# Kernel tuning notes

Hardware: AMD Instinct MI355X
Metric: run time of the kernel (lower is better)

Reference implementation:

```python
import jax, jax.numpy as jnp
import numpy as np
import math

B, T, C, H = 2, 1024, 1024, 16
D = C // H


def setup_inputs() -> dict:
    key = jax.random.key(0)
    ks = jax.random.split(key, 7)
    scale = 1.0 / math.sqrt(C)
    q = jax.random.normal(ks[0], (B, T, C), dtype=jnp.float32)
    k = jax.random.normal(ks[1], (B, T, C), dtype=jnp.float32)
    v = jax.random.normal(ks[2], (B, T, C), dtype=jnp.float32)
    # causal mask, True = masked out (matches create_causal_mask)
    mask = jnp.triu(jnp.ones((T, T), dtype=bool), k=1)[None, None]
    Wk = jax.random.normal(ks[3], (C, C), dtype=jnp.float32) * scale
    bk = jax.random.normal(ks[4], (C,), dtype=jnp.float32) * scale
    Wc = jax.random.normal(ks[5], (C, C), dtype=jnp.float32) * scale
    bc = jax.random.normal(ks[6], (C,), dtype=jnp.float32) * scale
    return {"q": q, "k": k, "v": v, "mask": mask, "Wk": Wk, "bk": bk, "Wc": Wc, "bc": bc}


def reference(q, k, v, mask, Wk, bk, Wc, bc):
    # NOTE: original module uses self.k_attn for ALL of q, k, v (q_attn/v_attn unused).
    qB, qT, qC = q.shape
    kT = k.shape[1]
    qp = (q @ Wk.T + bk).reshape(qB, qT, H, D).transpose(0, 2, 1, 3)  # [B,H,Tq,D]
    kp = (k @ Wk.T + bk).reshape(qB, kT, H, D).transpose(0, 2, 1, 3)  # [B,H,Tk,D]
    vp = (v @ Wk.T + bk).reshape(qB, kT, H, D).transpose(0, 2, 1, 3)  # [B,H,Tk,D]
    att = jnp.einsum('bhqd,bhkd->bhqk', qp, kp) * (1.0 / math.sqrt(D))
    att = jnp.where(mask, -jnp.inf, att)
    att = jax.nn.softmax(att, axis=-1)
    y = jnp.einsum('bhqk,bhkd->bhqd', att, vp)
    y = y.transpose(0, 2, 1, 3).reshape(qB, qT, qC)
    return y @ Wc.T + bc
```

## Files before the change

kernel.cpp:

```cpp
#include <hip/hip_runtime.h>

#define T_DIM 1024
#define C_DIM 1024
#define H_DIM 16
#define D_DIM 64
#define KD    1024

typedef short  short8  __attribute__((ext_vector_type(8)));
typedef short  short4v __attribute__((ext_vector_type(4)));
typedef float  f32x4   __attribute__((ext_vector_type(4)));

__device__ __forceinline__ float bf2f(short s) {
  return __uint_as_float(((unsigned)(unsigned short)s) << 16);
}
__device__ __forceinline__ short f2bf(float f) {
  unsigned u = __float_as_uint(f);
  u += 0x7fffu + ((u >> 16) & 1u);
  return (short)(u >> 16);
}
__device__ __forceinline__ unsigned pk2(float lo, float hi) {
  return ((unsigned)(unsigned short)f2bf(lo)) | (((unsigned)(unsigned short)f2bf(hi)) << 16);
}

__device__ __forceinline__ void gl2lds16(const short* g, short* l) {
  __builtin_amdgcn_global_load_lds(
      (const __attribute__((address_space(1))) unsigned int*)(const void*)g,
      (__attribute__((address_space(3))) unsigned int*)(void*)l,
      16, 0, 0);
}

__device__ __forceinline__ short8 ldfrag(const void* p, size_t off, int isf32) {
  if (isf32) {
    const float* q = (const float*)p + off;
    f32x4 lo = *(const f32x4*)q;
    f32x4 hi = *(const f32x4*)(q + 4);
    short8 r;
#pragma unroll
    for (int j = 0; j < 4; ++j) { r[j] = f2bf(lo[j]); r[j + 4] = f2bf(hi[j]); }
    return r;
  }
  return *(const short8*)((const short*)p + off);
}
__device__ __forceinline__ float ldbias(const void* b, int i, int isf32) {
  return isf32 ? ((const float*)b)[i] : bf2f(((const short*)b)[i]);
}

__device__ __forceinline__ int detect_f32_inblock(const unsigned* w, int lane) {
  int c = 0;
#pragma unroll
  for (int i = 0; i < 4; ++i) {
    unsigned e = (w[lane * 4 + i] >> 7) & 0xffu;
    c += (e >= 110u && e <= 135u) ? 1 : 0;
  }
#pragma unroll
  for (int off = 32; off; off >>= 1) c += __shfl_xor(c, off);
  return (c < 128) ? 1 : 0;
}

#define SZE  ((size_t)2 * T_DIM * C_DIM)
#define QN   ((size_t)2097152)
#define WN   ((size_t)1048576)
#define BN   ((size_t)1024)
#define CVT_TOT (3 * QN + 2 * WN + 2 * BN)

__global__ __launch_bounds__(256) void cvt_k(const void* __restrict__ q,
                                             const void* __restrict__ k,
                                             const void* __restrict__ v,
                                             const void* __restrict__ wk,
                                             const void* __restrict__ wc,
                                             const void* __restrict__ bk,
                                             const void* __restrict__ bc,
                                             short* __restrict__ dst)
{
  const int lane = threadIdx.x & 63;
  const int f = detect_f32_inblock((const unsigned*)q, lane);

  const size_t idx = (size_t)blockIdx.x * 1024 + threadIdx.x * 4;
  if (idx >= CVT_TOT) return;
  const void* src;
  size_t loc;
  if      (idx <     QN)          { src = q;  loc = idx; }
  else if (idx < 2 * QN)          { src = k;  loc = idx - QN; }
  else if (idx < 3 * QN)          { src = v;  loc = idx - 2 * QN; }
  else if (idx < 3 * QN + WN)     { src = wk; loc = idx - 3 * QN; }
  else if (idx < 3 * QN + 2 * WN) { src = wc; loc = idx - 3 * QN - WN; }
  else if (idx < 3 * QN + 2 * WN + BN) { src = bk; loc = idx - 3 * QN - 2 * WN; }
  else                            { src = bc; loc = idx - 3 * QN - 2 * WN - BN; }

  short4v o;
  if (f) {
    f32x4 x = *(const f32x4*)((const float*)src + loc);
#pragma unroll
    for (int j = 0; j < 4; ++j) o[j] = f2bf(x[j]);
  } else {
    o = *(const short4v*)((const short*)src + loc);
  }
  *(short4v*)(dst + idx) = o;
}

__device__ __forceinline__ void stage8x8(const short* gsrc, short* S, int R0,
                                         int lane, int koff) {
  const int rw = R0 + (lane >> 3);
  const int q  = (lane & 7) ^ (rw & 7);
  gl2lds16(gsrc + (size_t)rw * KD + koff + q * 8, &S[R0 * 64]);
}
__device__ __forceinline__ short8 fragread64(const short* S, int row, int chunk) {
  const int sl = (row << 3) + (chunk ^ (row & 7));
  return *(const short8*)&S[sl << 3];
}

__global__ __launch_bounds__(256) void gemm_qkv_a(const short* __restrict__ X0,
                                                  const short* __restrict__ X1,
                                                  const short* __restrict__ X2,
                                                  const short* __restrict__ Wv,
                                                  const short* __restrict__ Bv,
                                                  short* __restrict__ outv)
{
  const int tid  = threadIdx.x;
  const int lane = tid & 63;
  const int wave = tid >> 6;
  const int col16 = lane & 15;
  const int quad  = lane >> 4;

  const int f   = blockIdx.x;
  const int xcd = f & 7;
  const int j   = f >> 3;
  const int mt  = xcd * 6 + (j % 6);
  const int ct  = j / 6;
  const int m0 = mt * 128;
  const int c0 = ct * 64;

  const int src = m0 >> 11;
  const short* Xv = (src == 0) ? X0 : (src == 1) ? X1 : X2;
  const int arow = m0 & 2047;
  const bool isv = (src == 2);
  short* outb = outv + (size_t)src * SZE;

  __shared__ short As[2][128 * 64];
  __shared__ short Bs[2][64 * 64];

  const short* Xg = Xv + (size_t)arow * KD;
  const short* Wg = Wv + (size_t)c0 * KD;

  f32x4 acc[2][4] = {};

  stage8x8(Xg, As[0], wave * 32,      lane, 0);
  stage8x8(Xg, As[0], wave * 32 + 8,  lane, 0);
  stage8x8(Xg, As[0], wave * 32 + 16, lane, 0);
  stage8x8(Xg, As[0], wave * 32 + 24, lane, 0);
  stage8x8(Wg, Bs[0], wave * 16,      lane, 0);
  stage8x8(Wg, Bs[0], wave * 16 + 8,  lane, 0);
  __syncthreads();

  int cur = 0;
  for (int k0 = 0; k0 < KD; k0 += 64) {
    if (k0 + 64 < KD) {
      short* An = As[cur ^ 1];
      short* Bn = Bs[cur ^ 1];
      stage8x8(Xg, An, wave * 32,      lane, k0 + 64);
      stage8x8(Xg, An, wave * 32 + 8,  lane, k0 + 64);
      stage8x8(Xg, An, wave * 32 + 16, lane, k0 + 64);
      stage8x8(Xg, An, wave * 32 + 24, lane, k0 + 64);
      stage8x8(Wg, Bn, wave * 16,      lane, k0 + 64);
      stage8x8(Wg, Bn, wave * 16 + 8,  lane, k0 + 64);
    }

    const short* Ac = As[cur];
    const short* Bc = Bs[cur];
#pragma unroll
    for (int kk = 0; kk < 2; ++kk) {
      short8 fx[2], fw[4];
#pragma unroll
      for (int i = 0; i < 2; ++i)
        fx[i] = fragread64(Ac, wave * 32 + i * 16 + col16, kk * 4 + quad);
#pragma unroll
      for (int jj = 0; jj < 4; ++jj)
        fw[jj] = fragread64(Bc, jj * 16 + col16, kk * 4 + quad);

      if (isv) {
#pragma unroll
        for (int i = 0; i < 2; ++i)
#pragma unroll
          for (int jj = 0; jj < 4; ++jj)
            acc[i][jj] = __builtin_amdgcn_mfma_f32_16x16x32_bf16(fx[i], fw[jj], acc[i][jj], 0, 0, 0);
      } else {
#pragma unroll
        for (int i = 0; i < 2; ++i)
#pragma unroll
          for (int jj = 0; jj < 4; ++jj)
            acc[i][jj] = __builtin_amdgcn_mfma_f32_16x16x32_bf16(fw[jj], fx[i], acc[i][jj], 0, 0, 0);
      }
    }

    __syncthreads();
    cur ^= 1;
  }

  if (isv) {
#pragma unroll
    for (int i = 0; i < 2; ++i) {
#pragma unroll
      for (int jj = 0; jj < 4; ++jj) {
        const int c  = c0 + jj * 16 + col16;
        const int t0 = arow + wave * 32 + i * 16 + quad * 4;
        const float bv = bf2f(Bv[c]);
        short4v pk;
#pragma unroll
        for (int r = 0; r < 4; ++r) pk[r] = f2bf(acc[i][jj][r] + bv);
        const int bb = t0 >> 10, t = t0 & 1023, h = c >> 6, d = c & 63;
        size_t off = (size_t)((bb * H_DIM + h) * D_DIM + d) * T_DIM + t;
        *(short4v*)(outb + off) = pk;
      }
    }
  } else {
#pragma unroll
    for (int i = 0; i < 2; ++i) {
#pragma unroll
      for (int jj = 0; jj < 4; ++jj) {
        const int m  = arow + wave * 32 + i * 16 + col16;
        const int cb = c0 + jj * 16 + quad * 4;
        short4v bv4 = *(const short4v*)(Bv + cb);
        short4v pk;
#pragma unroll
        for (int r = 0; r < 4; ++r) pk[r] = f2bf(acc[i][jj][r] + bf2f(bv4[r]));
        const int bb = m >> 10, t = m & 1023, h = cb >> 6, d = cb & 63;
        size_t off = ((size_t)(bb * H_DIM + h) << 16) + (size_t)t * D_DIM + d;
        *(short4v*)(outb + off) = pk;
      }
    }
  }
}

__global__ __launch_bounds__(256) void gemm_out_a(const short* __restrict__ Xb,
                                                  const short* __restrict__ Wv,
                                                  const short* __restrict__ Bv,
                                                  float* __restrict__ outv)
{
  const int tid  = threadIdx.x;
  const int lane = tid & 63;
  const int wave = tid >> 6;
  const int col16 = lane & 15;
  const int quad  = lane >> 4;
  const int wm = wave & 1;
  const int wn = wave >> 1;

  const int f   = blockIdx.x;
  const int xcd = f & 7;
  const int j   = f >> 3;
  const int mt  = xcd * 4 + (j % 4);
  const int ct  = j / 4;
  const int m0 = mt * 64;
  const int c0 = ct * 64;

  __shared__ short As[2][64 * 64];
  __shared__ short Bs[2][64 * 64];

  const short* Xg = Xb + (size_t)m0 * KD;
  const short* Wg = Wv + (size_t)c0 * KD;

  f32x4 acc[2][2] = {};

  stage8x8(Xg, As[0], wave * 16,     lane, 0);
  stage8x8(Xg, As[0], wave * 16 + 8, lane, 0);
  stage8x8(Wg, Bs[0], wave * 16,     lane, 0);
  stage8x8(Wg, Bs[0], wave * 16 + 8, lane, 0);
  __syncthreads();

  int cur = 0;
  for (int k0 = 0; k0 < KD; k0 += 64) {
    if (k0 + 64 < KD) {
      short* An = As[cur ^ 1];
      short* Bn = Bs[cur ^ 1];
      stage8x8(Xg, An, wave * 16,     lane, k0 + 64);
      stage8x8(Xg, An, wave * 16 + 8, lane, k0 + 64);
      stage8x8(Wg, Bn, wave * 16,     lane, k0 + 64);
      stage8x8(Wg, Bn, wave * 16 + 8, lane, k0 + 64);
    }

    const short* Ac = As[cur];
    const short* Bc = Bs[cur];
#pragma unroll
    for (int kk = 0; kk < 2; ++kk) {
      short8 fx[2], fw[2];
#pragma unroll
      for (int i = 0; i < 2; ++i)
        fx[i] = fragread64(Ac, wm * 32 + i * 16 + col16, kk * 4 + quad);
#pragma unroll
      for (int jj = 0; jj < 2; ++jj)
        fw[jj] = fragread64(Bc, wn * 32 + jj * 16 + col16, kk * 4 + quad);

#pragma unroll
      for (int i = 0; i < 2; ++i)
#pragma unroll
        for (int jj = 0; jj < 2; ++jj)
          acc[i][jj] = __builtin_amdgcn_mfma_f32_16x16x32_bf16(fw[jj], fx[i], acc[i][jj], 0, 0, 0);
    }

    __syncthreads();
    cur ^= 1;
  }

#pragma unroll
  for (int i = 0; i < 2; ++i) {
#pragma unroll
    for (int jj = 0; jj < 2; ++jj) {
      const int m  = m0 + wm * 32 + i * 16 + col16;
      const int cb = c0 + wn * 32 + jj * 16 + quad * 4;
      f32x4 pv;
#pragma unroll
      for (int r = 0; r < 4; ++r) pv[r] = acc[i][jj][r] + bf2f(Bv[cb + r]);
      *(f32x4*)(outv + (size_t)m * C_DIM + cb) = pv;
    }
  }
}

#define LDSP 40

template<int KIND>
__global__ __launch_bounds__(256) void gemm2_k(const void* __restrict__ X0,
                                               const void* __restrict__ X1,
                                               const void* __restrict__ X2,
                                               const void* __restrict__ Wv,
                                               const void* __restrict__ Bv,
                                               void* __restrict__ outv)
{
  const int tid  = threadIdx.x;
  const int lane = tid & 63;
  const int wave = tid >> 6;
  const int col16 = lane & 15;
  const int quad  = lane >> 4;
  const int wm = wave & 1;
  const int wn = wave >> 1;

  const int f  = detect_f32_inblock((const unsigned*)Wv, lane);
  const int wf = f;
  const int xf = (KIND == 1) ? f : 0;

  const int m0 = blockIdx.x * 64;
  const int c0 = blockIdx.y * 64;

  const void* Xv = X0;
  int arow = m0;
  bool isv = false;
  short* outb = (short*)outv;
  if (KIND == 1) {
    const int src = m0 >> 11;
    Xv = (src == 0) ? X0 : (src == 1) ? X1 : X2;
    arow = m0 & 2047;
    isv = (src == 2);
    outb = (short*)outv + (size_t)src * SZE;
  }

  __shared__ short As[64 * LDSP];
  __shared__ short Bs[64 * LDSP];

  const int srow = tid >> 2;
  const int sc8  = tid & 3;

  f32x4 acc[2][2] = {};

  for (int k0 = 0; k0 < KD; k0 += 32) {
    short8 va = ldfrag(Xv, (size_t)(arow + srow) * KD + k0 + sc8 * 8, xf);
    short8 vb = ldfrag(Wv, (size_t)(c0 + srow) * KD + k0 + sc8 * 8, wf);
    if (k0) __syncthreads();
    *(short8*)&As[srow * LDSP + sc8 * 8] = va;
    *(short8*)&Bs[srow * LDSP + sc8 * 8] = vb;
    __syncthreads();

    short8 fx[2], fw[2];
#pragma unroll
    for (int i = 0; i < 2; ++i)
      fx[i] = *(const short8*)&As[(wm * 32 + i * 16 + col16) * LDSP + quad * 8];
#pragma unroll
    for (int jj = 0; jj < 2; ++jj)
      fw[jj] = *(const short8*)&Bs[(wn * 32 + jj * 16 + col16) * LDSP + quad * 8];

    if (KIND == 1 && isv) {
#pragma unroll
      for (int i = 0; i < 2; ++i)
#pragma unroll
        for (int jj = 0; jj < 2; ++jj)
          acc[i][jj] = __builtin_amdgcn_mfma_f32_16x16x32_bf16(fx[i], fw[jj], acc[i][jj], 0, 0, 0);
    } else {
#pragma unroll
      for (int i = 0; i < 2; ++i)
#pragma unroll
        for (int jj = 0; jj < 2; ++jj)
          acc[i][jj] = __builtin_amdgcn_mfma_f32_16x16x32_bf16(fw[jj], fx[i], acc[i][jj], 0, 0, 0);
    }
  }

  if (KIND == 1 && isv) {
#pragma unroll
    for (int i = 0; i < 2; ++i) {
#pragma unroll
      for (int jj = 0; jj < 2; ++jj) {
        const int c  = c0 + wn * 32 + jj * 16 + col16;
        const int t0 = arow + wm * 32 + i * 16 + quad * 4;
        const float bv = ldbias(Bv, c, wf);
        short4v pk;
#pragma unroll
        for (int r = 0; r < 4; ++r) pk[r] = f2bf(acc[i][jj][r] + bv);
        const int bb = t0 >> 10, t = t0 & 1023, h = c >> 6, d = c & 63;
        size_t off = (size_t)((bb * H_DIM + h) * D_DIM + d) * T_DIM + t;
        *(short4v*)(outb + off) = pk;
      }
    }
  } else {
#pragma unroll
    for (int i = 0; i < 2; ++i) {
#pragma unroll
      for (int jj = 0; jj < 2; ++jj) {
        const int m  = arow + wm * 32 + i * 16 + col16;
        const int cb = c0 + wn * 32 + jj * 16 + quad * 4;
        if (KIND == 0) {
          f32x4 pv;
#pragma unroll
          for (int r = 0; r < 4; ++r) pv[r] = acc[i][jj][r] + ldbias(Bv, cb + r, wf);
          *(f32x4*)((float*)outv + (size_t)m * C_DIM + cb) = pv;
        } else {
          short4v pk;
#pragma unroll
          for (int r = 0; r < 4; ++r) pk[r] = f2bf(acc[i][jj][r] + ldbias(Bv, cb + r, wf));
          const int bb = m >> 10, t = m & 1023, h = cb >> 6, d = cb & 63;
          size_t off = ((size_t)(bb * H_DIM + h) << 16) + (size_t)t * D_DIM + d;
          *(short4v*)(outb + off) = pk;
        }
      }
    }
  }
}

__global__ __launch_bounds__(256) void attn_k3(const short* __restrict__ qp,
                                               const short* __restrict__ kp,
                                               const short* __restrict__ vpt,
                                               short* __restrict__ y)
{
  const int lane = threadIdx.x & 63;
  const int wave = threadIdx.x >> 6;
  const int col  = lane & 15;
  const int quad = lane >> 4;
  const int bh = blockIdx.x;
  const int b = bh >> 4, h = bh & 15;
  const int qt = 63 - (int)blockIdx.y;
  const int q0 = qt * 16;
  const int myq = q0 + col;

  const short* qph = qp  + (size_t)bh * (T_DIM * D_DIM);
  const short* kph = kp  + (size_t)bh * (T_DIM * D_DIM);
  const short* vph = vpt + (size_t)bh * (D_DIM * T_DIM);

  const int nkt  = (q0 + 47) >> 5;
  const int base = nkt >> 2, rem = nkt & 3;
  const int cnt   = base + (wave < rem ? 1 : 0);
  const int start = wave * base + (wave < rem ? wave : rem);

  short8 bQ[2];
#pragma unroll
  for (int kk = 0; kk < 2; ++kk)
    bQ[kk] = *(const short8*)(qph + (size_t)(q0 + col) * D_DIM + kk * 32 + quad * 8);

  f32x4 O[4] = {};
  float rs = 0.0f;

  const int slA = col + ((quad & 1) * 32);
  const int slB = slA + 16;

  short8 cK0a, cK0b;
  {
    const short* p0 = kph + (size_t)(start * 32 + col) * D_DIM + quad * 8;
    cK0a = *(const short8*)(p0);
    cK0b = *(const short8*)(p0 + 32);
  }

#pragma unroll 1
  for (int kt = start; kt < start + cnt; ++kt) {
    const int kb = kt * 32;

    const short* kb1 = kph + (size_t)(kb + 16 + col) * D_DIM + quad * 8;
    short8 aK1a = *(const short8*)(kb1);
    short8 aK1b = *(const short8*)(kb1 + 32);
    const short* nb0 = kph + (size_t)(kb + 32 + col) * D_DIM + quad * 8;
    short8 nK0a = *(const short8*)(nb0);
    short8 nK0b = *(const short8*)(nb0 + 32);

    f32x4 st[2];
    {
      f32x4 s = {0.f, 0.f, 0.f, 0.f};
      __builtin_amdgcn_s_setprio(1);
      s = __builtin_amdgcn_mfma_f32_16x16x32_bf16(cK0a, bQ[0], s, 0, 0, 0);
      s = __builtin_amdgcn_mfma_f32_16x16x32_bf16(cK0b, bQ[1], s, 0, 0, 0);
      st[0] = s;
      f32x4 t = {0.f, 0.f, 0.f, 0.f};
      t = __builtin_amdgcn_mfma_f32_16x16x32_bf16(aK1a, bQ[0], t, 0, 0, 0);
      t = __builtin_amdgcn_mfma_f32_16x16x32_bf16(aK1b, bQ[1], t, 0, 0, 0);
      __builtin_amdgcn_s_setprio(0);
      st[1] = t;
    }

#pragma unroll
    for (int jt = 0; jt < 2; ++jt) {
#pragma unroll
      for (int r = 0; r < 4; ++r) {
        const int key = kb + jt * 16 + quad * 4 + r;
        float p = __expf(st[jt][r] * 0.125f);
        p = (key > myq) ? 0.0f : p;
        st[jt][r] = p;
        rs += p;
      }
    }

    short8 aV[4];
#pragma unroll
    for (int dt = 0; dt < 4; ++dt)
      aV[dt] = *(const short8*)(vph + (size_t)(dt * 16 + col) * T_DIM + kb + quad * 8);

    const int a0 = (int)pk2(st[0][0], st[0][1]);
    const int a1 = (int)pk2(st[0][2], st[0][3]);
    const int b0 = (int)pk2(st[1][0], st[1][1]);
    const int b1 = (int)pk2(st[1][2], st[1][3]);
    const int tA0 = __shfl(a0, slA, 64), tB0 = __shfl(b0, slA, 64);
    const int tA1 = __shfl(a1, slA, 64), tB1 = __shfl(b1, slA, 64);
    const int tA2 = __shfl(a0, slB, 64), tB2 = __shfl(b0, slB, 64);
    const int tA3 = __shfl(a1, slB, 64), tB3 = __shfl(b1, slB, 64);
    union { unsigned u[4]; short8 s8; } uu;
    uu.u[0] = (unsigned)((quad < 2) ? tA0 : tB0);
    uu.u[1] = (unsigned)((quad < 2) ? tA1 : tB1);
    uu.u[2] = (unsigned)((quad < 2) ? tA2 : tB2);
    uu.u[3] = (unsigned)((quad < 2) ? tA3 : tB3);
    const short8 bP32 = uu.s8;

    __builtin_amdgcn_s_setprio(1);
#pragma unroll
    for (int dt = 0; dt < 4; ++dt)
      O[dt] = __builtin_amdgcn_mfma_f32_16x16x32_bf16(aV[dt], bP32, O[dt], 0, 0, 0);
    __builtin_amdgcn_s_setprio(0);

    cK0a = nK0a;
    cK0b = nK0b;
  }

  rs += __shfl_xor(rs, 16);
  rs += __shfl_xor(rs, 32);

  __shared__ float Om[4 * 4 * 16 * 16];
  __shared__ float Ll[4][16];

#pragma unroll
  for (int dt = 0; dt < 4; ++dt)
    *(f32x4*)&Om[((wave * 4 + dt) * 4 + quad) * 64 + col * 4] = O[dt];
  if (quad == 0) Ll[wave][col] = rs;
  __syncthreads();

  float L = Ll[0][col] + Ll[1][col] + Ll[2][col] + Ll[3][col];
  f32x4 oacc = {0.f, 0.f, 0.f, 0.f};
#pragma unroll
  for (int w = 0; w < 4; ++w) {
    f32x4 ov = *(const f32x4*)&Om[((w * 4 + wave) * 4 + quad) * 64 + col * 4];
#pragma unroll
    for (int r = 0; r < 4; ++r) oacc[r] += ov[r];
  }
  const float rl = 1.0f / L;
  const int t = q0 + col;
  const size_t ybase = ((size_t)(b * T_DIM + t)) * C_DIM + h * D_DIM + quad * 4;
  short4v pk;
#pragma unroll
  for (int r = 0; r < 4; ++r) pk[r] = f2bf(oacc[r] * rl);
  *(short4v*)(y + ybase + wave * 16) = pk;
}

extern "C" void kernel_launch(void* const* d_in, const int* in_sizes, int n_in,
                              void* d_out, int out_size, void* d_ws, size_t ws_size,
                              hipStream_t stream) {
  const void* q = d_in[0];
  const void* k = d_in[1];
  const void* v = d_in[2];
  int wi = (n_in >= 8 && in_sizes[4] == C_DIM * C_DIM) ? 4 : 3;
  const void* Wk = d_in[wi];
  const void* bk = d_in[wi + 1];
  const void* Wc = d_in[wi + 2];
  const void* bc = d_in[wi + 3];

  short* ws  = (short*)d_ws;
  short* qp  = ws;
  short* kp  = ws + SZE;
  short* vpt = ws + 2 * SZE;
  short* y   = ws + 3 * SZE;

  short* ext = ws + 4 * SZE;
  const size_t needed = (4 * SZE + CVT_TOT) * sizeof(short);
  const bool pre = (ws_size >= needed);

  dim3 blk(256);
  if (pre) {
    cvt_k<<<dim3((unsigned)((CVT_TOT + 1023) / 1024)), blk, 0, stream>>>(
        q, k, v, Wk, Wc, bk, bc, ext);
    const short* gq  = ext;
    const short* gk  = ext + QN;
    const short* gv  = ext + 2 * QN;
    const short* gwk = ext + 3 * QN;
    const short* gwc = ext + 3 * QN + WN;
    const short* gbk = ext + 3 * QN + 2 * WN;
    const short* gbc = ext + 3 * QN + 2 * WN + BN;

    gemm_qkv_a<<<dim3(768), blk, 0, stream>>>(gq, gk, gv, gwk, gbk, qp);
    attn_k3<<<dim3(32, 64), blk, 0, stream>>>(qp, kp, vpt, y);
    gemm_out_a<<<dim3(512), blk, 0, stream>>>(y, gwc, gbc, (float*)d_out);
  } else {
    gemm2_k<1><<<dim3(96, 16), blk, 0, stream>>>(q, k, v, Wk, bk, qp);
    attn_k3<<<dim3(32, 64), blk, 0, stream>>>(qp, kp, vpt, y);
    gemm2_k<0><<<dim3(32, 16), blk, 0, stream>>>(y, nullptr, nullptr, Wc, bc, d_out);
  }
}
```

Before: 161.1 us.

## Assign one query tile per wave with balanced pairing, drop split-K reduction

```diff
diff --git a/kernel.cpp b/kernel.cpp
--- a/kernel.cpp
+++ b/kernel.cpp
@@ -431,7 +431,7 @@
   }
 }
 
-__global__ __launch_bounds__(256) void attn_k3(const short* __restrict__ qp,
+__global__ __launch_bounds__(256) void attn_k4(const short* __restrict__ qp,
                                                const short* __restrict__ kp,
                                                const short* __restrict__ vpt,
                                                short* __restrict__ y)
@@ -442,7 +442,11 @@
   const int quad = lane >> 4;
   const int bh = blockIdx.x;
   const int b = bh >> 4, h = bh & 15;
-  const int qt = 63 - (int)blockIdx.y;
+  const int g = (int)blockIdx.y;
+  const int qt = (wave == 0) ? 2 * g
+               : (wave == 1) ? 63 - 2 * g
+               : (wave == 2) ? 2 * g + 1
+               :               62 - 2 * g;
   const int q0 = qt * 16;
   const int myq = q0 + col;
 
@@ -450,10 +454,7 @@
   const short* kph = kp  + (size_t)bh * (T_DIM * D_DIM);
   const short* vph = vpt + (size_t)bh * (D_DIM * T_DIM);
 
-  const int nkt  = (q0 + 47) >> 5;
-  const int base = nkt >> 2, rem = nkt & 3;
-  const int cnt   = base + (wave < rem ? 1 : 0);
-  const int start = wave * base + (wave < rem ? wave : rem);
+  const int cnt = (q0 + 47) >> 5;
 
   short8 bQ[2];
 #pragma unroll
@@ -468,13 +469,13 @@
 
   short8 cK0a, cK0b;
   {
-    const short* p0 = kph + (size_t)(start * 32 + col) * D_DIM + quad * 8;
+    const short* p0 = kph + (size_t)(col) * D_DIM + quad * 8;
     cK0a = *(const short8*)(p0);
     cK0b = *(const short8*)(p0 + 32);
   }
 
 #pragma unroll 1
-  for (int kt = start; kt < start + cnt; ++kt) {
+  for (int kt = 0; kt < cnt; ++kt) {
     const int kb = kt * 32;
 
     const short* kb1 = kph + (size_t)(kb + 16 + col) * D_DIM + quad * 8;
@@ -542,31 +543,17 @@
 
   rs += __shfl_xor(rs, 16);
   rs += __shfl_xor(rs, 32);
-
-  __shared__ float Om[4 * 4 * 16 * 16];
-  __shared__ float Ll[4][16];
-
-#pragma unroll
-  for (int dt = 0; dt < 4; ++dt)
-    *(f32x4*)&Om[((wave * 4 + dt) * 4 + quad) * 64 + col * 4] = O[dt];
-  if (quad == 0) Ll[wave][col] = rs;
-  __syncthreads();
-
-  float L = Ll[0][col] + Ll[1][col] + Ll[2][col] + Ll[3][col];
-  f32x4 oacc = {0.f, 0.f, 0.f, 0.f};
-#pragma unroll
-  for (int w = 0; w < 4; ++w) {
-    f32x4 ov = *(const f32x4*)&Om[((w * 4 + wave) * 4 + quad) * 64 + col * 4];
-#pragma unroll
-    for (int r = 0; r < 4; ++r) oacc[r] += ov[r];
-  }
-  const float rl = 1.0f / L;
+  const float rl = 1.0f / rs;
+
   const int t = q0 + col;
   const size_t ybase = ((size_t)(b * T_DIM + t)) * C_DIM + h * D_DIM + quad * 4;
-  short4v pk;
-#pragma unroll
-  for (int r = 0; r < 4; ++r) pk[r] = f2bf(oacc[r] * rl);
-  *(short4v*)(y + ybase + wave * 16) = pk;
+#pragma unroll
+  for (int dt = 0; dt < 4; ++dt) {
+    short4v pk;
+#pragma unroll
+    for (int r = 0; r < 4; ++r) pk[r] = f2bf(O[dt][r] * rl);
+    *(short4v*)(y + ybase + dt * 16) = pk;
+  }
 }
 
 extern "C" void kernel_launch(void* const* d_in, const int* in_sizes, int n_in,
@@ -604,11 +591,11 @@
     const short* gbc = ext + 3 * QN + 2 * WN + BN;
 
     gemm_qkv_a<<<dim3(768), blk, 0, stream>>>(gq, gk, gv, gwk, gbk, qp);
-    attn_k3<<<dim3(32, 64), blk, 0, stream>>>(qp, kp, vpt, y);
+    attn_k4<<<dim3(32, 16), blk, 0, stream>>>(qp, kp, vpt, y);
     gemm_out_a<<<dim3(512), blk, 0, stream>>>(y, gwc, gbc, (float*)d_out);
   } else {
     gemm2_k<1><<<dim3(96, 16), blk, 0, stream>>>(q, k, v, Wk, bk, qp);
-    attn_k3<<<dim3(32, 64), blk, 0, stream>>>(qp, kp, vpt, y);
+    attn_k4<<<dim3(32, 16), blk, 0, stream>>>(qp, kp, vpt, y);
     gemm2_k<0><<<dim3(32, 16), blk, 0, stream>>>(y, nullptr, nullptr, Wc, bc, d_out);
   }
 }
```

After: 156.6 us. 1.03x faster.
